# Kernel optimization log

Hardware: AMD Instinct MI355X
Metric: run time of the kernel (lower is better)

Reference implementation:

```python
import jax, jax.numpy as jnp
import numpy as np

B, S, I, H, O = 64, 512, 256, 1024, 128

def setup_inputs() -> dict:
    key = jax.random.key(0)
    ks = jax.random.split(key, 9)
    s_in = 1.0 / np.sqrt(I)
    s_h = 1.0 / np.sqrt(H)
    return {
        "x": jax.random.normal(ks[0], (B, S, I), dtype=jnp.float32),
        "W_in": jax.random.uniform(ks[1], (H, I), jnp.float32, -s_in, s_in),
        "b_in": jax.random.uniform(ks[2], (H,), jnp.float32, -s_in, s_in),
        "W_rec": jax.random.uniform(ks[3], (H, H), jnp.float32, -s_h, s_h),
        "b_rec": jax.random.uniform(ks[4], (H,), jnp.float32, -s_h, s_h),
        "tau_m": jnp.full((H,), 2.0, dtype=jnp.float32),
        "tau_n": jnp.full((H,), 2.0, dtype=jnp.float32),
        "W_out": jax.random.uniform(ks[5], (O, H), jnp.float32, -s_h, s_h),
        "b_out": jax.random.uniform(ks[6], (O,), jnp.float32, -s_h, s_h),
    }

def reference(x, W_in, b_in, W_rec, b_rec, tau_m, tau_n, W_out, b_out):
    b, s, _ = x.shape
    h = W_in.shape[0]
    alpha = jax.nn.sigmoid(tau_m)  # [H]
    beta = jax.nn.sigmoid(tau_n)   # [H]
    # Precompute feedforward GEMM for all timesteps at once: [B,S,H]
    ff = jnp.einsum('bsi,hi->bsh', x, W_in) + b_in

    def step(carry, ff_t):
        mem, d, prev_spike = carry  # each [B,H]
        total = ff_t + prev_spike @ W_rec.T + b_rec
        d = beta * d + (1.0 - beta) * total
        mem = alpha * mem + (1.0 - alpha) * d
        spike = (mem > 1.0).astype(mem.dtype)
        mem = mem * (1.0 - spike)
        out = jax.nn.sigmoid(spike @ W_out.T + b_out)  # [B,O]
        return (mem, d, spike), out

    zeros = jnp.zeros((b, h), dtype=x.dtype)
    _, outs = jax.lax.scan(step, (zeros, zeros, zeros), jnp.swapaxes(ff, 0, 1))
    return jnp.swapaxes(outs, 0, 1)  # [B,S,O]
```

## Files before the change

### kernel.cpp

```cpp
#include <hip/hip_runtime.h>
#include <hip/hip_bf16.h>
#include <stdint.h>

#define B_ 64
#define S_ 512
#define I_ 256
#define H_ 1024
#define O_ 128
#define M_ (B_*S_)
#define ST_ 1032

typedef float f32x4 __attribute__((ext_vector_type(4)));
typedef unsigned short u16x4 __attribute__((ext_vector_type(4)));

__device__ __forceinline__ unsigned short f2bf(float f) {
    unsigned u = __float_as_uint(f);
    u += 0x7FFFu + ((u >> 16) & 1u);
    return (unsigned short)(u >> 16);
}
__device__ __forceinline__ float bf2f(unsigned short s) {
    return __uint_as_float((unsigned)s << 16);
}

__global__ void __launch_bounds__(256) k0_convert(
    const float* __restrict__ x, const float* __restrict__ Win,
    const float* __restrict__ tau_m, const float* __restrict__ tau_n,
    uint8_t* __restrict__ xf8, uint8_t* __restrict__ wf8,
    unsigned* __restrict__ firstCross, unsigned* __restrict__ cnt)
{
    __shared__ unsigned lds32[32 * 65];
    const int i = blockIdx.x;
    const int t = threadIdx.x;

    const float* src;
    uint8_t* dstBase;
    int kqStride;
    if (i < 1024) {
        src = x + (size_t)(i * 32) * 256;
        dstBase = xf8 + (size_t)(i >> 2) * 32768 + (i & 3) * 2 * 512;
        kqStride = 4096;
    } else {
        const int i2 = i - 1024;
        src = Win + (size_t)(i2 * 32) * 256;
        dstBase = wf8 + (size_t)(i2 >> 1) * 16384 + (i2 & 1) * 2 * 512;
        kqStride = 2048;
    }

#pragma unroll
    for (int j = 0; j < 8; ++j) {
        const int f = j * 256 + t;
        const int lrow = f >> 6, c4 = f & 63;
        float4 v = *(const float4*)(src + (size_t)lrow * 256 + c4 * 4);
        int w0 = 0;
        w0 = __builtin_amdgcn_cvt_pk_fp8_f32(v.x, v.y, w0, false);
        w0 = __builtin_amdgcn_cvt_pk_fp8_f32(v.z, v.w, w0, true);
        lds32[lrow * 65 + c4] = (unsigned)w0;
    }
    __syncthreads();

#pragma unroll
    for (int j = 0; j < 2; ++j) {
        const int c = j * 256 + t;
        const int kq  = c >> 6;
        const int rbl = (c >> 5) & 1;
        const int l0  = (c & 31) * 2;
        const int r   = l0 & 15;
        const int q   = l0 >> 4;
        const int lrow = rbl * 16 + r;
        const int c0 = kq * 8 + q * 2;
        uint4 o;
        o.x = lds32[lrow * 65 + c0];
        o.y = lds32[lrow * 65 + c0 + 1];
        o.z = lds32[(lrow + 1) * 65 + c0];
        o.w = lds32[(lrow + 1) * 65 + c0 + 1];
        *(uint4*)(dstBase + kq * kqStride + rbl * 512 + l0 * 8) = o;
    }

    if (i == 0) {
        if (t < 64) firstCross[t] = 0xFFFFFFFFu;
        else if (t < 128) cnt[t - 64] = 0u;
        __syncthreads();
        bool bad = false;
        for (int j = t; j < H_; j += 256) {
            float a  = 1.f / (1.f + expf(-tau_m[j]));
            float be = 1.f / (1.f + expf(-tau_n[j]));
            float g  = fmaxf(a, be);
            float bound = __powf(g, 64.f) * (1.f + 64.f * (1.f - g)) * 8.f;
            if (!(bound < 0.1f) || !(g < 1.f) || !(g >= 0.f)) bad = true;
        }
        if (bad)
            for (int b2 = 0; b2 < 64; ++b2) atomicMin(firstCross + b2, 0u);
    }
}

__global__ void __launch_bounds__(256) kf_gemm_scan(
    const uint8_t* __restrict__ xf8, const uint8_t* __restrict__ wf8,
    const float* __restrict__ b_in, const float* __restrict__ b_rec,
    const float* __restrict__ tau_m, const float* __restrict__ tau_n,
    const float* __restrict__ b_out,
    unsigned* __restrict__ firstCross, unsigned* __restrict__ cnt,
    float* __restrict__ out)
{
    __shared__ uint8_t lS[64 * ST_];
    __shared__ int lastFlag;

    const int tid  = threadIdx.x;
    const int w    = tid >> 6;
    const int lane = tid & 63;
    const int idx  = blockIdx.x;
    const int b    = (idx & 7) | ((idx >> 7) << 3);
    const int hn   = (idx >> 3) & 15;
    const int colrow = lane & 15;
    const int quad   = lane >> 4;

    const uint8_t* wB = wf8 + (size_t)hn * 16384 + lane * 8;
    long long bq[32];
#pragma unroll
    for (int kq = 0; kq < 8; ++kq)
#pragma unroll
        for (int ni = 0; ni < 4; ++ni)
            bq[kq * 4 + ni] = *(const long long*)(wB + kq * 2048 + ni * 512);

    for (int tt = 0; tt < 4; ++tt) {
        const uint8_t* xA = xf8 + (size_t)(b * 4 + tt) * 32768
                          + w * 1024 + lane * 8;
        long long a[16];
#pragma unroll
        for (int kq = 0; kq < 8; ++kq) {
            a[kq * 2]     = *(const long long*)(xA + kq * 4096);
            a[kq * 2 + 1] = *(const long long*)(xA + kq * 4096 + 512);
        }
        f32x4 acc[2][4];
#pragma unroll
        for (int mi = 0; mi < 2; ++mi)
#pragma unroll
            for (int ni = 0; ni < 4; ++ni)
                acc[mi][ni] = (f32x4){0.f, 0.f, 0.f, 0.f};
#pragma unroll
        for (int kq = 0; kq < 8; ++kq)
#pragma unroll
            for (int mi = 0; mi < 2; ++mi)
#pragma unroll
                for (int ni = 0; ni < 4; ++ni)
                    acc[mi][ni] = __builtin_amdgcn_mfma_f32_16x16x32_fp8_fp8(
                        a[kq * 2 + mi], bq[kq * 4 + ni], acc[mi][ni], 0, 0, 0);

#pragma unroll
        for (int mi = 0; mi < 2; ++mi) {
            const int T0 = tt * 128 + w * 32 + mi * 16 + quad * 4;
            const int gb = ((T0 >> 3) << 4) + ((T0 & 7) << 1);
#pragma unroll
            for (int ni = 0; ni < 4; ++ni) {
                const int h0 = ni * 16 + colrow;
                u16x4 p;
                p[0] = f2bf(acc[mi][ni][0]);
                p[1] = f2bf(acc[mi][ni][1]);
                p[2] = f2bf(acc[mi][ni][2]);
                p[3] = f2bf(acc[mi][ni][3]);
                *(u16x4*)(lS + h0 * ST_ + gb) = p;
            }
        }
    }
    __syncthreads();

    {
        const int h = tid & 63;
        const int c = tid >> 6;
        const int hs = hn * 64 + h;
        const float alpha = 1.f / (1.f + expf(-tau_m[hs]));
        const float beta  = 1.f / (1.f + expf(-tau_n[hs]));
        const float oma = 1.f - alpha, omb = 1.f - beta;
        const float bsum = b_in[hs] + b_rec[hs];

        const int t0     = (c == 0) ? 0 : (c * 128 - 64);
        const int nsteps = (c == 0) ? 128 : 192;
        const int ckFrom = (c == 0) ? 0 : 64;

        const uint8_t* row = lS + h * ST_;
        float d = 0.f, mem = 0.f;
        bool flag = false;
        for (int s = 0; s < nsteps; s += 4) {
            const int T = t0 + s;
            u16x4 v = *(const u16x4*)(row + ((T >> 3) << 4) + ((T & 7) << 1));
            const bool chk = (s >= ckFrom);
#pragma unroll
            for (int u = 0; u < 4; ++u) {
                const float tot = bf2f(v[u]) + bsum;
                d   = fmaf(beta,  d,   omb * tot);
                mem = fmaf(alpha, mem, oma * d);
                if (chk && (mem > 0.8f || fabsf(tot) > 8.f)) flag = true;
            }
        }
        if (__ballot(flag)) {
            if (lane == 0) atomicMin(firstCross + b, 0u);
        }
    }

    __syncthreads();
    if (tid == 0) {
        __threadfence();
        unsigned old = atomicAdd(cnt + b, 1u);
        int flag = 0;
        if (old == 15u) {
            __threadfence();
            unsigned fc = atomicAdd(firstCross + b, 0u);
            flag = (fc == 0xFFFFFFFFu) ? 1 : 0;
        }
        lastFlag = flag;
    }
    __syncthreads();
    if (lastFlag) {
        float* sg = (float*)lS;
        if (tid < 128) sg[tid] = 1.f / (1.f + expf(-b_out[tid]));
        __syncthreads();
        const int q = tid & 31;
        float4 v = *(float4*)(sg + q * 4);
        float* obase = out + (size_t)b * (S_ * O_) + q * 4;
        const int trow = tid >> 5;
#pragma unroll 4
        for (int k = 0; k < 64; ++k)
            *(float4*)(obase + (size_t)(trow + k * 8) * O_) = v;
    }
}

__global__ void __launch_bounds__(1024) k3_repair(
    const float* __restrict__ x, const float* __restrict__ W_in,
    const float* __restrict__ b_in,
    const float* __restrict__ W_rec, const float* __restrict__ b_rec,
    const float* __restrict__ tau_m, const float* __restrict__ tau_n,
    const float* __restrict__ W_out, const float* __restrict__ b_out,
    const unsigned* __restrict__ firstCross,
    unsigned long long* __restrict__ gmask,
    float* __restrict__ out)
{
    const int b = blockIdx.x;
    if (firstCross[b] == 0xFFFFFFFFu) return;
    const int h = threadIdx.x;
    __shared__ float xrow[I_];
    __shared__ unsigned long long msk[16];
    if (h < 16) msk[h] = 0ull;
    const float alpha = 1.f / (1.f + expf(-tau_m[h]));
    const float beta  = 1.f / (1.f + expf(-tau_n[h]));
    const float bsum  = b_in[h] + b_rec[h];
    const float* wi = W_in + (size_t)h * I_;
    const float* wr = W_rec + (size_t)h * H_;
    float d = 0.f, mem = 0.f;
    for (int t = 0; t < S_; ++t) {
        __syncthreads();
        if (h < I_) xrow[h] = x[((size_t)b * S_ + t) * I_ + h];
        __syncthreads();
        float ffv = 0.f;
        for (int k = 0; k < I_; ++k) ffv += xrow[k] * wi[k];
        float rec = 0.f;
#pragma unroll
        for (int wd = 0; wd < 16; ++wd) {
            unsigned long long mw = msk[wd];
            while (mw) {
                int bit = __ffsll((long long)mw) - 1;
                rec += wr[(wd << 6) + bit];
                mw &= (mw - 1);
            }
        }
        float tot = ffv + bsum + rec;
        d   = beta  * d   + (1.f - beta)  * tot;
        mem = alpha * mem + (1.f - alpha) * d;
        int sp = (mem > 1.0f) ? 1 : 0;
        if (sp) mem = 0.f;
        unsigned long long bal = __ballot(sp);
        __syncthreads();
        if ((h & 63) == 0) {
            msk[h >> 6] = bal;
            gmask[((size_t)b * S_ + t) * 16 + (h >> 6)] = bal;
        }
    }
    __syncthreads();
    __threadfence_block();
    for (int i = h; i < S_ * O_; i += 1024) {
        const int t = i >> 7, o = i & (O_ - 1);
        float logit = b_out[o];
        const unsigned long long* m = gmask + ((size_t)b * S_ + t) * 16;
        const float* wo = W_out + (size_t)o * H_;
        for (int wd = 0; wd < 16; ++wd) {
            unsigned long long mw = m[wd];
            while (mw) {
                int bit = __ffsll((long long)mw) - 1;
                logit += wo[(wd << 6) + bit];
                mw &= (mw - 1);
            }
        }
        out[((size_t)b * S_ + t) * O_ + o] = 1.f / (1.f + expf(-logit));
    }
}

extern "C" void kernel_launch(void* const* d_in, const int* in_sizes, int n_in,
                              void* d_out, int out_size, void* d_ws, size_t ws_size,
                              hipStream_t stream) {
    const float* x     = (const float*)d_in[0];
    const float* W_in  = (const float*)d_in[1];
    const float* b_in  = (const float*)d_in[2];
    const float* W_rec = (const float*)d_in[3];
    const float* b_rec = (const float*)d_in[4];
    const float* tau_m = (const float*)d_in[5];
    const float* tau_n = (const float*)d_in[6];
    const float* W_out = (const float*)d_in[7];
    const float* b_out = (const float*)d_in[8];
    float* out = (float*)d_out;

    char* ws = (char*)d_ws;
    size_t off = 0;
    uint8_t* xf8 = (uint8_t*)(ws + off);               off += (size_t)M_ * I_;
    uint8_t* wf8 = (uint8_t*)(ws + off);               off += (size_t)H_ * I_;
    unsigned long long* gmask = (unsigned long long*)(ws + off); off += (size_t)B_ * S_ * 16 * 8;
    unsigned* firstCross = (unsigned*)(ws + off);      off += 256;
    unsigned* cnt = (unsigned*)(ws + off);             off += 256;
    if (ws_size < off) return;

    k0_convert<<<1056, 256, 0, stream>>>(x, W_in, tau_m, tau_n, xf8, wf8,
                                         firstCross, cnt);
    kf_gemm_scan<<<1024, 256, 0, stream>>>(xf8, wf8, b_in, b_rec, tau_m, tau_n,
                                           b_out, firstCross, cnt, out);
    k3_repair<<<64, 1024, 0, stream>>>(x, W_in, b_in, W_rec, b_rec, tau_m, tau_n,
                                       W_out, b_out, firstCross, gmask, out);
}
```

Before: 150.1 us.

## Coarsen GEMM-scan blocks, stage FP8 weights in LDS, split constant-output write

The fused FP8 GEMM and screening-scan kernel now runs 256 blocks instead of 1024. Each block loads a 64 KB quarter of the converted W_in into LDS with global_load_lds and loops over four 64-column chunks, so weights are reused across chunks rather than reloaded into registers per block. The convert kernel is coarsened the same way, with each block handling four 32-row tiles. The atomic last-block counter that wrote the constant sigmoid(b_out) output is replaced by a separate k4_out kernel gated on firstCross. The risks are an extra launch, roughly 130 KB of LDS per block limiting occupancy to one block per CU, and more serial work per block.

```diff
diff --git a/kernel.cpp b/kernel.cpp
--- a/kernel.cpp
+++ b/kernel.cpp
@@ -26,59 +26,62 @@
     const float* __restrict__ x, const float* __restrict__ Win,
     const float* __restrict__ tau_m, const float* __restrict__ tau_n,
     uint8_t* __restrict__ xf8, uint8_t* __restrict__ wf8,
-    unsigned* __restrict__ firstCross, unsigned* __restrict__ cnt)
+    unsigned* __restrict__ firstCross)
 {
     __shared__ unsigned lds32[32 * 65];
     const int i = blockIdx.x;
     const int t = threadIdx.x;
 
-    const float* src;
-    uint8_t* dstBase;
-    int kqStride;
-    if (i < 1024) {
-        src = x + (size_t)(i * 32) * 256;
-        dstBase = xf8 + (size_t)(i >> 2) * 32768 + (i & 3) * 2 * 512;
-        kqStride = 4096;
-    } else {
-        const int i2 = i - 1024;
-        src = Win + (size_t)(i2 * 32) * 256;
-        dstBase = wf8 + (size_t)(i2 >> 1) * 16384 + (i2 & 1) * 2 * 512;
-        kqStride = 2048;
-    }
-
-#pragma unroll
-    for (int j = 0; j < 8; ++j) {
-        const int f = j * 256 + t;
-        const int lrow = f >> 6, c4 = f & 63;
-        float4 v = *(const float4*)(src + (size_t)lrow * 256 + c4 * 4);
-        int w0 = 0;
-        w0 = __builtin_amdgcn_cvt_pk_fp8_f32(v.x, v.y, w0, false);
-        w0 = __builtin_amdgcn_cvt_pk_fp8_f32(v.z, v.w, w0, true);
-        lds32[lrow * 65 + c4] = (unsigned)w0;
-    }
-    __syncthreads();
-
-#pragma unroll
-    for (int j = 0; j < 2; ++j) {
-        const int c = j * 256 + t;
-        const int kq  = c >> 6;
-        const int rbl = (c >> 5) & 1;
-        const int l0  = (c & 31) * 2;
-        const int r   = l0 & 15;
-        const int q   = l0 >> 4;
-        const int lrow = rbl * 16 + r;
-        const int c0 = kq * 8 + q * 2;
-        uint4 o;
-        o.x = lds32[lrow * 65 + c0];
-        o.y = lds32[lrow * 65 + c0 + 1];
-        o.z = lds32[(lrow + 1) * 65 + c0];
-        o.w = lds32[(lrow + 1) * 65 + c0 + 1];
-        *(uint4*)(dstBase + kq * kqStride + rbl * 512 + l0 * 8) = o;
+    for (int j2 = 0; j2 < 4; ++j2) {
+        const float* src;
+        uint8_t* dstBase;
+        int kqStride;
+        if (i < 256) {
+            const int r0 = i * 128 + j2 * 32;
+            src = x + (size_t)r0 * 256;
+            dstBase = xf8 + (size_t)i * 32768 + (size_t)(j2 * 2) * 512;
+            kqStride = 4096;
+        } else {
+            const int r0 = (i - 256) * 128 + j2 * 32;
+            src = Win + (size_t)r0 * 256;
+            dstBase = wf8 + (size_t)(r0 >> 6) * 16384 + (size_t)((j2 & 1) * 2) * 512;
+            kqStride = 2048;
+        }
+        if (j2) __syncthreads();
+
+#pragma unroll
+        for (int j = 0; j < 8; ++j) {
+            const int f = j * 256 + t;
+            const int lrow = f >> 6, c4 = f & 63;
+            float4 v = *(const float4*)(src + (size_t)lrow * 256 + c4 * 4);
+            int w0 = 0;
+            w0 = __builtin_amdgcn_cvt_pk_fp8_f32(v.x, v.y, w0, false);
+            w0 = __builtin_amdgcn_cvt_pk_fp8_f32(v.z, v.w, w0, true);
+            lds32[lrow * 65 + c4] = (unsigned)w0;
+        }
+        __syncthreads();
+
+#pragma unroll
+        for (int j = 0; j < 2; ++j) {
+            const int c = j * 256 + t;
+            const int kq  = c >> 6;
+            const int rbl = (c >> 5) & 1;
+            const int l0  = (c & 31) * 2;
+            const int r   = l0 & 15;
+            const int q   = l0 >> 4;
+            const int lrow = rbl * 16 + r;
+            const int c0 = kq * 8 + q * 2;
+            uint4 o;
+            o.x = lds32[lrow * 65 + c0];
+            o.y = lds32[lrow * 65 + c0 + 1];
+            o.z = lds32[(lrow + 1) * 65 + c0];
+            o.w = lds32[(lrow + 1) * 65 + c0 + 1];
+            *(uint4*)(dstBase + kq * kqStride + rbl * 512 + l0 * 8) = o;
+        }
     }
 
     if (i == 0) {
         if (t < 64) firstCross[t] = 0xFFFFFFFFu;
-        else if (t < 128) cnt[t - 64] = 0u;
         __syncthreads();
         bool bad = false;
         for (int j = t; j < H_; j += 256) {
@@ -97,129 +100,113 @@
     const uint8_t* __restrict__ xf8, const uint8_t* __restrict__ wf8,
     const float* __restrict__ b_in, const float* __restrict__ b_rec,
     const float* __restrict__ tau_m, const float* __restrict__ tau_n,
-    const float* __restrict__ b_out,
-    unsigned* __restrict__ firstCross, unsigned* __restrict__ cnt,
-    float* __restrict__ out)
+    unsigned* __restrict__ firstCross)
 {
+    __shared__ uint8_t lB[65536];
     __shared__ uint8_t lS[64 * ST_];
-    __shared__ int lastFlag;
 
     const int tid  = threadIdx.x;
     const int w    = tid >> 6;
     const int lane = tid & 63;
     const int idx  = blockIdx.x;
-    const int b    = (idx & 7) | ((idx >> 7) << 3);
-    const int hn   = (idx >> 3) & 15;
+    const int b    = (idx & 7) | ((idx >> 5) << 3);
+    const int hq   = (idx >> 3) & 3;
     const int colrow = lane & 15;
     const int quad   = lane >> 4;
 
-    const uint8_t* wB = wf8 + (size_t)hn * 16384 + lane * 8;
-    long long bq[32];
-#pragma unroll
-    for (int kq = 0; kq < 8; ++kq)
-#pragma unroll
-        for (int ni = 0; ni < 4; ++ni)
-            bq[kq * 4 + ni] = *(const long long*)(wB + kq * 2048 + ni * 512);
-
-    for (int tt = 0; tt < 4; ++tt) {
-        const uint8_t* xA = xf8 + (size_t)(b * 4 + tt) * 32768
-                          + w * 1024 + lane * 8;
-        long long a[16];
-#pragma unroll
-        for (int kq = 0; kq < 8; ++kq) {
-            a[kq * 2]     = *(const long long*)(xA + kq * 4096);
-            a[kq * 2 + 1] = *(const long long*)(xA + kq * 4096 + 512);
-        }
-        f32x4 acc[2][4];
-#pragma unroll
-        for (int mi = 0; mi < 2; ++mi)
-#pragma unroll
-            for (int ni = 0; ni < 4; ++ni)
-                acc[mi][ni] = (f32x4){0.f, 0.f, 0.f, 0.f};
-#pragma unroll
-        for (int kq = 0; kq < 8; ++kq)
+    const uint8_t* gB = wf8 + (size_t)hq * 65536;
+#pragma unroll
+    for (int j = 0; j < 16; ++j) {
+        const int off = j * 4096 + tid * 16;
+        __builtin_amdgcn_global_load_lds(
+            (const __attribute__((address_space(1))) void*)(gB + off),
+            (__attribute__((address_space(3))) void*)(lB + off), 16, 0, 0);
+    }
+    __syncthreads();
+
+    bool flag = false;
+
+    for (int hn = 0; hn < 4; ++hn) {
+        for (int tt = 0; tt < 4; ++tt) {
+            const uint8_t* xA = xf8 + (size_t)(b * 4 + tt) * 32768
+                              + w * 1024 + lane * 8;
+            long long a[16];
+#pragma unroll
+            for (int kq = 0; kq < 8; ++kq) {
+                a[kq * 2]     = *(const long long*)(xA + kq * 4096);
+                a[kq * 2 + 1] = *(const long long*)(xA + kq * 4096 + 512);
+            }
+            f32x4 acc[2][4];
 #pragma unroll
             for (int mi = 0; mi < 2; ++mi)
 #pragma unroll
                 for (int ni = 0; ni < 4; ++ni)
-                    acc[mi][ni] = __builtin_amdgcn_mfma_f32_16x16x32_fp8_fp8(
-                        a[kq * 2 + mi], bq[kq * 4 + ni], acc[mi][ni], 0, 0, 0);
-
-#pragma unroll
-        for (int mi = 0; mi < 2; ++mi) {
-            const int T0 = tt * 128 + w * 32 + mi * 16 + quad * 4;
-            const int gb = ((T0 >> 3) << 4) + ((T0 & 7) << 1);
-#pragma unroll
-            for (int ni = 0; ni < 4; ++ni) {
-                const int h0 = ni * 16 + colrow;
-                u16x4 p;
-                p[0] = f2bf(acc[mi][ni][0]);
-                p[1] = f2bf(acc[mi][ni][1]);
-                p[2] = f2bf(acc[mi][ni][2]);
-                p[3] = f2bf(acc[mi][ni][3]);
-                *(u16x4*)(lS + h0 * ST_ + gb) = p;
-            }
-        }
-    }
-    __syncthreads();
-
-    {
-        const int h = tid & 63;
-        const int c = tid >> 6;
-        const int hs = hn * 64 + h;
-        const float alpha = 1.f / (1.f + expf(-tau_m[hs]));
-        const float beta  = 1.f / (1.f + expf(-tau_n[hs]));
-        const float oma = 1.f - alpha, omb = 1.f - beta;
-        const float bsum = b_in[hs] + b_rec[hs];
-
-        const int t0     = (c == 0) ? 0 : (c * 128 - 64);
-        const int nsteps = (c == 0) ? 128 : 192;
-        const int ckFrom = (c == 0) ? 0 : 64;
-
-        const uint8_t* row = lS + h * ST_;
-        float d = 0.f, mem = 0.f;
-        bool flag = false;
-        for (int s = 0; s < nsteps; s += 4) {
-            const int T = t0 + s;
-            u16x4 v = *(const u16x4*)(row + ((T >> 3) << 4) + ((T & 7) << 1));
-            const bool chk = (s >= ckFrom);
-#pragma unroll
-            for (int u = 0; u < 4; ++u) {
-                const float tot = bf2f(v[u]) + bsum;
-                d   = fmaf(beta,  d,   omb * tot);
-                mem = fmaf(alpha, mem, oma * d);
-                if (chk && (mem > 0.8f || fabsf(tot) > 8.f)) flag = true;
-            }
-        }
-        if (__ballot(flag)) {
-            if (lane == 0) atomicMin(firstCross + b, 0u);
-        }
-    }
-
-    __syncthreads();
-    if (tid == 0) {
-        __threadfence();
-        unsigned old = atomicAdd(cnt + b, 1u);
-        int flag = 0;
-        if (old == 15u) {
-            __threadfence();
-            unsigned fc = atomicAdd(firstCross + b, 0u);
-            flag = (fc == 0xFFFFFFFFu) ? 1 : 0;
-        }
-        lastFlag = flag;
-    }
-    __syncthreads();
-    if (lastFlag) {
-        float* sg = (float*)lS;
-        if (tid < 128) sg[tid] = 1.f / (1.f + expf(-b_out[tid]));
-        __syncthreads();
-        const int q = tid & 31;
-        float4 v = *(float4*)(sg + q * 4);
-        float* obase = out + (size_t)b * (S_ * O_) + q * 4;
-        const int trow = tid >> 5;
-#pragma unroll 4
-        for (int k = 0; k < 64; ++k)
-            *(float4*)(obase + (size_t)(trow + k * 8) * O_) = v;
+                    acc[mi][ni] = (f32x4){0.f, 0.f, 0.f, 0.f};
+#pragma unroll
+            for (int kq = 0; kq < 8; ++kq) {
+                long long bfr[4];
+#pragma unroll
+                for (int ni = 0; ni < 4; ++ni)
+                    bfr[ni] = *(const long long*)(lB + hn * 16384 + kq * 2048
+                                                  + ni * 512 + lane * 8);
+#pragma unroll
+                for (int mi = 0; mi < 2; ++mi)
+#pragma unroll
+                    for (int ni = 0; ni < 4; ++ni)
+                        acc[mi][ni] = __builtin_amdgcn_mfma_f32_16x16x32_fp8_fp8(
+                            a[kq * 2 + mi], bfr[ni], acc[mi][ni], 0, 0, 0);
+            }
+#pragma unroll
+            for (int mi = 0; mi < 2; ++mi) {
+                const int T0 = tt * 128 + w * 32 + mi * 16 + quad * 4;
+                const int gb = ((T0 >> 3) << 4) + ((T0 & 7) << 1);
+#pragma unroll
+                for (int ni = 0; ni < 4; ++ni) {
+                    const int h0 = ni * 16 + colrow;
+                    u16x4 p;
+                    p[0] = f2bf(acc[mi][ni][0]);
+                    p[1] = f2bf(acc[mi][ni][1]);
+                    p[2] = f2bf(acc[mi][ni][2]);
+                    p[3] = f2bf(acc[mi][ni][3]);
+                    *(u16x4*)(lS + h0 * ST_ + gb) = p;
+                }
+            }
+        }
+        __syncthreads();
+
+        {
+            const int h = tid & 63;
+            const int c = tid >> 6;
+            const int hs = (hq * 4 + hn) * 64 + h;
+            const float alpha = 1.f / (1.f + expf(-tau_m[hs]));
+            const float beta  = 1.f / (1.f + expf(-tau_n[hs]));
+            const float oma = 1.f - alpha, omb = 1.f - beta;
+            const float bsum = b_in[hs] + b_rec[hs];
+
+            const int t0     = (c == 0) ? 0 : (c * 128 - 64);
+            const int nsteps = (c == 0) ? 128 : 192;
+            const int ckFrom = (c == 0) ? 0 : 64;
+
+            const uint8_t* row = lS + h * ST_;
+            float d = 0.f, mem = 0.f;
+            for (int s = 0; s < nsteps; s += 4) {
+                const int T = t0 + s;
+                u16x4 v = *(const u16x4*)(row + ((T >> 3) << 4) + ((T & 7) << 1));
+                const bool chk = (s >= ckFrom);
+#pragma unroll
+                for (int u = 0; u < 4; ++u) {
+                    const float tot = bf2f(v[u]) + bsum;
+                    d   = fmaf(beta,  d,   omb * tot);
+                    mem = fmaf(alpha, mem, oma * d);
+                    if (chk && (mem > 0.8f || fabsf(tot) > 8.f)) flag = true;
+                }
+            }
+        }
+        __syncthreads();
+    }
+
+    if (__ballot(flag)) {
+        if (lane == 0) atomicMin(firstCross + b, 0u);
     }
 }
 
@@ -292,6 +279,24 @@
     }
 }
 
+__global__ void __launch_bounds__(256) k4_out(
+    const float* __restrict__ b_out,
+    const unsigned* __restrict__ firstCross,
+    float* __restrict__ out)
+{
+    const int i4 = blockIdx.x * 256 + threadIdx.x;
+    const int b  = i4 >> 14;
+    if (firstCross[b] != 0xFFFFFFFFu) return;
+    const int o4 = i4 & 31;
+    float4 v = *(const float4*)(b_out + o4 * 4);
+    float4 r;
+    r.x = 1.f / (1.f + expf(-v.x));
+    r.y = 1.f / (1.f + expf(-v.y));
+    r.z = 1.f / (1.f + expf(-v.z));
+    r.w = 1.f / (1.f + expf(-v.w));
+    *(float4*)(out + (size_t)i4 * 4) = r;
+}
+
 extern "C" void kernel_launch(void* const* d_in, const int* in_sizes, int n_in,
                               void* d_out, int out_size, void* d_ws, size_t ws_size,
                               hipStream_t stream) {
@@ -312,13 +317,12 @@
     uint8_t* wf8 = (uint8_t*)(ws + off);               off += (size_t)H_ * I_;
     unsigned long long* gmask = (unsigned long long*)(ws + off); off += (size_t)B_ * S_ * 16 * 8;
     unsigned* firstCross = (unsigned*)(ws + off);      off += 256;
-    unsigned* cnt = (unsigned*)(ws + off);             off += 256;
     if (ws_size < off) return;
 
-    k0_convert<<<1056, 256, 0, stream>>>(x, W_in, tau_m, tau_n, xf8, wf8,
-                                         firstCross, cnt);
-    kf_gemm_scan<<<1024, 256, 0, stream>>>(xf8, wf8, b_in, b_rec, tau_m, tau_n,
-                                           b_out, firstCross, cnt, out);
+    k0_convert<<<264, 256, 0, stream>>>(x, W_in, tau_m, tau_n, xf8, wf8, firstCross);
+    kf_gemm_scan<<<256, 256, 0, stream>>>(xf8, wf8, b_in, b_rec, tau_m, tau_n,
+                                          firstCross);
     k3_repair<<<64, 1024, 0, stream>>>(x, W_in, b_in, W_rec, b_rec, tau_m, tau_n,
                                        W_out, b_out, firstCross, gmask, out);
-}
+    k4_out<<<4096, 256, 0, stream>>>(b_out, firstCross, out);
+}
```

New measurement: 162.0 us. 1.08x slower.
